# Performance work log

Measured on AMD Instinct MI355X. Metric: run time of the kernel, lower is better.

The kernel has to match this reference:

```python
import math
import jax, jax.numpy as jnp
import numpy as np

B, S, D, H = 4, 1024, 512, 8
DK = D // H


def lin(x, W, b):
    # torch nn.Linear: y = x @ W.T + b, W: [out, in]
    return jnp.einsum('...i,oi->...o', x, W) + b


def layer_norm(x, scale, bias, eps=1e-5):
    m = jnp.mean(x, axis=-1, keepdims=True)
    v = jnp.var(x, axis=-1, keepdims=True)
    return (x - m) / jnp.sqrt(v + eps) * scale + bias


def mha(q_in, k_in, v_in, Wq, bq, Wk, bk, Wv, bv, Wo, bo, gammas, mask, zero_pad):
    b, s, _ = q_in.shape
    q = lin(q_in, Wq, bq).reshape(b, s, H, DK).transpose(0, 2, 1, 3)  # bhsd
    k = lin(k_in, Wk, bk).reshape(b, s, H, DK).transpose(0, 2, 1, 3)
    v = lin(v_in, Wv, bv).reshape(b, s, H, DK).transpose(0, 2, 1, 3)
    scores = jnp.einsum('bhid,bhjd->bhij', q, k) / math.sqrt(DK)
    # no-grad distance-decay branch
    s_ = jnp.where(mask, scores, jnp.float32(-1e32))
    s_ = jax.nn.softmax(s_, axis=-1) * mask
    distcum = jnp.cumsum(s_, axis=-1)
    disttotal = jnp.sum(s_, axis=-1, keepdims=True)
    idx = jnp.arange(s)
    pos = jnp.abs(idx[None, :] - idx[:, None]).astype(jnp.float32)[None, None]  # |i-j|
    dist = jax.lax.stop_gradient(jnp.sqrt(jnp.clip((disttotal - distcum) * pos, 0.0, None)))
    gamma = -jax.nn.softplus(gammas)[None]  # [1,h,1,1]
    total_effect = jnp.clip(jnp.exp(dist * gamma), 1e-5, 1e5)
    scores = scores * total_effect
    # NOTE: original code calls scores.masked_fill(...) without assignment (no-op);
    # faithfully NOT re-masking before this softmax.
    att = jax.nn.softmax(scores, axis=-1)
    if zero_pad:
        att = att.at[:, :, 0, :].set(0.0)
    out = jnp.einsum('bhij,bhjd->bhid', att, v).transpose(0, 2, 1, 3).reshape(b, s, D)
    return lin(out, Wo, bo)


def setup_inputs() -> dict:
    key = jax.random.key(0)
    ks = jax.random.split(key, 32)
    ki = iter(range(32))

    def w(shape, scale=0.02):
        return jax.random.normal(ks[next(ki)], shape, jnp.float32) * scale

    inp = {
        'q_emb': jax.random.normal(ks[next(ki)], (B, S, D), jnp.float32),
        'qa_emb': jax.random.normal(ks[next(ki)], (B, S, D), jnp.float32),
    }
    for blk in (1, 2, 3):
        inp[f'Wq{blk}'] = w((D, D)); inp[f'bq{blk}'] = jnp.zeros((D,), jnp.float32)
        if blk == 3:
            inp['Wk3'] = w((D, D)); inp['bk3'] = jnp.zeros((D,), jnp.float32)
        inp[f'Wv{blk}'] = w((D, D)); inp[f'bv{blk}'] = jnp.zeros((D,), jnp.float32)
        inp[f'Wo{blk}'] = w((D, D)); inp[f'bo{blk}'] = jnp.zeros((D,), jnp.float32)
        inp[f'g{blk}'] = w((H, 1, 1), 0.5)
        inp[f'ls{blk}'] = jnp.ones((D,), jnp.float32)
        inp[f'lb{blk}'] = jnp.zeros((D,), jnp.float32)
    inp['know'] = jax.random.uniform(ks[next(ki)], (1, 1, D), jnp.float32, -1.0, 1.0)
    inp['Wlk'] = w((D, DK)); inp['b_lk'] = jnp.zeros((D,), jnp.float32)
    inp['Wlv'] = w((D, DK)); inp['b_lv'] = jnp.zeros((D,), jnp.float32)
    return inp


def reference(q_emb, qa_emb,
              Wq1, bq1, Wv1, bv1, Wo1, bo1, g1, ls1, lb1,
              Wq2, bq2, Wv2, bv2, Wo2, bo2, g2, ls2, lb2,
              Wq3, bq3, Wk3, bk3, Wv3, bv3, Wo3, bo3, g3, ls3, lb3,
              know, Wlk, b_lk, Wlv, b_lv):
    b, s, d = q_emb.shape
    ones = jnp.ones((s, s), dtype=bool)
    mask_peek = jnp.tril(ones, k=0)[None, None]   # peek_cur=True
    mask_nopeek = jnp.tril(ones, k=-1)[None, None]  # peek_cur=False

    # block1 / block2 share k and q projections (kq_same=True)
    hq = layer_norm(q_emb + mha(q_emb, q_emb, q_emb, Wq1, bq1, Wq1, bq1,
                                Wv1, bv1, Wo1, bo1, g1, mask_peek, False), ls1, lb1)
    ha = layer_norm(qa_emb + mha(qa_emb, qa_emb, qa_emb, Wq2, bq2, Wq2, bq2,
                                 Wv2, bv2, Wo2, bo2, g2, mask_peek, False), ls2, lb2)
    query = jnp.broadcast_to(know, (b, s, d))
    h = layer_norm(query + mha(query, hq, ha, Wq3, bq3, Wk3, bk3,
                               Wv3, bv3, Wo3, bo3, g3, mask_nopeek, True), ls3, lb3)

    # small multi-head combine
    key_t = jax.nn.sigmoid(lin(query.reshape(b, s, H, DK), Wlk, b_lk))  # [b,s,h,d]
    val_t = jax.nn.sigmoid(lin(h.reshape(b, s, H, DK), Wlv, b_lv))     # [b,s,h,d]
    beta = jnp.einsum('bshd,bsd->bsh', key_t, q_emb)
    alpha = jax.nn.softmax(beta, axis=-1)
    out = jnp.einsum('bsh,bshd->bsd', alpha, val_t)
    return out
```

## Files before the change

### kernel.cpp

```cpp
#include <hip/hip_runtime.h>
#include <math.h>

#define BB 4
#define S 1024
#define D 512
#define H 8
#define DKH 64

#define ATT_LD 1032
#define LOG2E 1.4426950408889634f

typedef __attribute__((ext_vector_type(8))) short bf16x8;
typedef __attribute__((ext_vector_type(4))) float f32x4;

#if __has_builtin(__builtin_amdgcn_exp2f)
#define EXP2(x) __builtin_amdgcn_exp2f(x)
#else
#define EXP2(x) exp2f(x)
#endif
#if __has_builtin(__builtin_amdgcn_sqrtf)
#define SQRTF(x) __builtin_amdgcn_sqrtf(x)
#else
#define SQRTF(x) sqrtf(x)
#endif
#if __has_builtin(__builtin_amdgcn_rcpf)
#define RCPF(x) __builtin_amdgcn_rcpf(x)
#else
#define RCPF(x) (1.0f / (x))
#endif

__device__ __forceinline__ unsigned short f2bf(float f){
  unsigned int u = __float_as_uint(f);
  u += 0x7FFFu + ((u >> 16) & 1u);
  return (unsigned short)(u >> 16);
}
__device__ __forceinline__ unsigned short f2bf_rhu(float f){
  return (unsigned short)((__float_as_uint(f) + 0x8000u) >> 16);
}
__device__ __forceinline__ unsigned int pk_rhu(float lo, float hi){
  unsigned int a = __float_as_uint(lo) + 0x8000u;
  unsigned int b = __float_as_uint(hi) + 0x8000u;
#if __has_builtin(__builtin_amdgcn_perm)
  return __builtin_amdgcn_perm(b, a, 0x07060302u);
#else
  return (a >> 16) | (b & 0xffff0000u);
#endif
}
__device__ __forceinline__ float bf2f(unsigned int v){
  return __uint_as_float(v << 16);
}
__device__ __forceinline__ f32x4 MFMA(bf16x8 a, bf16x8 b, f32x4 c){
  return __builtin_amdgcn_mfma_f32_16x16x32_bf16(a, b, c, 0, 0, 0);
}
__device__ __forceinline__ void gl_lds16(const void* g, void* l){
  __builtin_amdgcn_global_load_lds(
      (const __attribute__((address_space(1))) void*)g,
      (__attribute__((address_space(3))) void*)l, 16, 0, 0);
}

template<int CTRL>
__device__ __forceinline__ float dppadd(float v){
  int s = __builtin_amdgcn_update_dpp(0, __float_as_int(v), CTRL, 0xf, 0xf, true);
  return v + __int_as_float(s);
}
__device__ __forceinline__ float rdl(float v, int l){
  return __int_as_float(__builtin_amdgcn_readlane(__float_as_int(v), l));
}
__device__ __forceinline__ void wave_scan64(float v, int lane, float& incl, float& total){
  float r = dppadd<0x111>(v);
  r = dppadd<0x112>(r);
  r = dppadd<0x114>(r);
  r = dppadd<0x118>(r);
  float t0 = rdl(r, 15), t1 = rdl(r, 31), t2 = rdl(r, 47), t3 = rdl(r, 63);
  const int row = lane >> 4;
  float off = (row > 0 ? t0 : 0.f) + (row > 1 ? t1 : 0.f) + (row > 2 ? t2 : 0.f);
  incl = r + off;
  total = (t0 + t1) + (t2 + t3);
}
__device__ __forceinline__ float wave_sum64(float v){
  float r = dppadd<0x111>(v);
  r = dppadd<0x112>(r);
  r = dppadd<0x114>(r);
  r = dppadd<0x118>(r);
  return (rdl(r, 15) + rdl(r, 31)) + (rdl(r, 47) + rdl(r, 63));
}

__device__ __forceinline__ float blk_sum(float* r, int t, float v){
  r[t] = v; __syncthreads();
  for (int s = 128; s > 0; s >>= 1){
    if (t < s) r[t] += r[t + s];
    __syncthreads();
  }
  float res = r[0]; __syncthreads();
  return res;
}

struct GemmJobs {
  const unsigned short* A[4];
  const unsigned short* W[4];
  const float* bias[4];
  void* C[4];
};
template<int OUTBF>
__global__ __launch_bounds__(256) void mfma_gemm_b(GemmJobs jb)
{
  __shared__ __align__(16) short As[128][32];
  __shared__ __align__(16) short Ws[128][32];
  const int t = threadIdx.x;
  const int z = blockIdx.z;
  const int n0 = blockIdx.x * 128, m0 = blockIdx.y * 128;
  const unsigned short* A = jb.A[z];
  const unsigned short* W = jb.W[z];
  const float* bias = jb.bias[z];
  const int w = t >> 6, lane = t & 63;
  const int wm = (w >> 1) << 6, wn = (w & 1) << 6;
  const int lm = lane & 15, q = lane >> 4;
  const int r = t >> 2, cc = (t & 3) << 3;
  char* ldsA = ((char*)&As[0][0]) + w * 1024;
  char* ldsW = ((char*)&Ws[0][0]) + w * 1024;
  f32x4 acc[4][4];
  #pragma unroll
  for (int a_ = 0; a_ < 4; a_++)
    #pragma unroll
    for (int b_ = 0; b_ < 4; b_++)
      acc[a_][b_] = (f32x4){0.f, 0.f, 0.f, 0.f};
  for (int k0 = 0; k0 < D; k0 += 32){
    gl_lds16(&A[(size_t)(m0 + r)      * D + k0 + cc], ldsA);
    gl_lds16(&A[(size_t)(m0 + r + 64) * D + k0 + cc], ldsA + 4096);
    gl_lds16(&W[(size_t)(n0 + r)      * D + k0 + cc], ldsW);
    gl_lds16(&W[(size_t)(n0 + r + 64) * D + k0 + cc], ldsW + 4096);
    __syncthreads();
    bf16x8 af[4], bf[4];
    #pragma unroll
    for (int mt = 0; mt < 4; mt++) af[mt] = *(const bf16x8*)&As[wm + mt*16 + lm][q*8];
    #pragma unroll
    for (int nt = 0; nt < 4; nt++) bf[nt] = *(const bf16x8*)&Ws[wn + nt*16 + lm][q*8];
    #pragma unroll
    for (int mt = 0; mt < 4; mt++)
      #pragma unroll
      for (int nt = 0; nt < 4; nt++)
        acc[mt][nt] = MFMA(af[mt], bf[nt], acc[mt][nt]);
    __syncthreads();
  }
  #pragma unroll
  for (int nt = 0; nt < 4; nt++){
    const int n = n0 + wn + nt*16 + lm;
    const float bs = bias[n];
    #pragma unroll
    for (int mt = 0; mt < 4; mt++){
      const int mb = m0 + wm + mt*16 + (q << 2);
      f32x4 c = acc[mt][nt];
      #pragma unroll
      for (int rr = 0; rr < 4; rr++){
        float vv = c[rr] + bs;
        if (OUTBF)
          ((unsigned short*)jb.C[z])[(size_t)(mb + rr) * D + n] = f2bf(vv);
        else
          ((float*)jb.C[z])[(size_t)(mb + rr) * D + n] = vv;
      }
    }
  }
}

#define KS_LD 66
struct VTArgs { const unsigned short* v[2]; unsigned short* vt[2]; int nz; };
__global__ __launch_bounds__(256) void vt_kernel(VTArgs a)
{
  __shared__ unsigned short tile[64 * KS_LD];
  const int lin = blockIdx.x;
  const int xcd = lin & 7, slot = lin >> 3;
  const int j0 = (slot & 15) * 64;
  const int set = slot >> 4;
  const int z   = (a.nz == 2) ? (set & 1)  : 0;
  const int grp = (a.nz == 2) ? (set >> 1) : set;
  const int bh = xcd + 8 * grp, b = bh >> 3, h = bh & 7;
  const int t = threadIdx.x;
  const unsigned short* vp = a.v[z];
  unsigned short* vtp = a.vt[z] + (size_t)bh * 64 * S;
  #pragma unroll
  for (int p = 0; p < 2; p++){
    int lin2 = t + p * 256, row = lin2 >> 3, c8 = (lin2 & 7) << 3;
    *(uint4*)&tile[row * KS_LD + c8] =
      *(const uint4*)&vp[((size_t)b * S + j0 + row) * D + h * DKH + c8];
  }
  __syncthreads();
  #pragma unroll
  for (int p = 0; p < 2; p++){
    int lin2 = t + p * 256, d = lin2 >> 3, c8 = (lin2 & 7) << 3;
    unsigned short tmp[8];
    #pragma unroll
    for (int jx = 0; jx < 8; jx++) tmp[jx] = tile[(c8 + jx) * KS_LD + d];
    *(uint4*)&vtp[(size_t)d * S + j0 + c8] = *(const uint4*)tmp;
  }
}

struct FAArgs {
  const unsigned short* qk[2];
  const unsigned short* vt[2];
  unsigned short* ctx[2];
  const float* g[2];
  const float* c3;
  int diag, zero_pad, nz;
};
template<int C3>
__global__ __launch_bounds__(256, 4) void fused_attn(FAArgs a)
{
  __shared__ __align__(16) unsigned short att[16 * ATT_LD];
  __shared__ float ls2s[16];
  const int t = threadIdx.x;
  const int lin = blockIdx.x;
  const int xcd = lin & 7;
  const int slot = lin >> 3;
  const int i0 = (slot & 63) * 16;
  const int set = slot >> 6;
  const int z   = (a.nz == 2) ? (set & 1)  : 0;
  const int grp = (a.nz == 2) ? (set >> 1) : set;
  const int bh = xcd + 8 * grp, b = bh >> 3, h = bh & 7;
  const int w = t >> 6, lane = t & 63, lm = lane & 15, q = lane >> 4;
  const unsigned short* qkp = a.qk[z];
  const unsigned short* vtp = a.vt[z] + (size_t)bh * 64 * S;
  unsigned short* ctxp = a.ctx[z];
  float gm2;
  { float gv = a.g[z][h];
    gm2 = -((gv > 20.f) ? gv : log1pf(expf(gv))) * LOG2E; }

  if (!C3){
    const size_t rowbase = (size_t)b * S;
    bf16x8 af0 = *(const bf16x8*)&qkp[(rowbase + i0 + lm) * D + h * DKH + q*8];
    bf16x8 af1 = *(const bf16x8*)&qkp[(rowbase + i0 + lm) * D + h * DKH + 32 + q*8];
    size_t kb = (rowbase + w*16 + lm) * D + h * DKH;
    bf16x8 bv0 = *(const bf16x8*)&qkp[kb + q*8];
    bf16x8 bv1 = *(const bf16x8*)&qkp[kb + 32 + q*8];
    for (int jc = 0; jc < S; jc += 64){
      bf16x8 nb0, nb1;
      if (jc + 64 < S){
        size_t kb2 = (rowbase + jc + 64 + w*16 + lm) * D + h * DKH;
        nb0 = *(const bf16x8*)&qkp[kb2 + q*8];
        nb1 = *(const bf16x8*)&qkp[kb2 + 32 + q*8];
      }
      f32x4 acc = (f32x4){0.f, 0.f, 0.f, 0.f};
      acc = MFMA(af0, bv0, acc);
      acc = MFMA(af1, bv1, acc);
      #pragma unroll
      for (int rr = 0; rr < 4; rr++)
        att[(q*4 + rr) * ATT_LD + jc + w*16 + lm] = f2bf_rhu(acc[rr] * 0.125f);
      bv0 = nb0; bv1 = nb1;
    }
  }
  __syncthreads();

  const int jA0 = lane * 8, jB0 = 512 + lane * 8;

  float cH[16], erH[16];
  if (C3){
    const float* c3p = a.c3 + ((size_t)b * H + h) * S;
    #pragma unroll
    for (int sg = 0; sg < 2; sg++)
      #pragma unroll
      for (int p4 = 0; p4 < 2; p4++){
        float4 x = *(const float4*)&c3p[sg*512 + lane*8 + p4*4];
        cH[sg*8+p4*4+0] = x.x * LOG2E; cH[sg*8+p4*4+1] = x.y * LOG2E;
        cH[sg*8+p4*4+2] = x.z * LOG2E; cH[sg*8+p4*4+3] = x.w * LOG2E;
      }
    #pragma unroll
    for (int k = 0; k < 16; k++) erH[k] = EXP2(cH[k]);
  }

  auto decay_row = [&](const float (&c)[16], const float (&er)[16],
                       const int i, unsigned short* rowp, const int rl){
    const int jmax = i + a.diag;
    const bool skipB = (jmax < 512);
    float pl[16];
    float runA = 0.f;
    #pragma unroll
    for (int k = 0; k < 8; k++){
      float e = (jA0 + k <= jmax) ? er[k] : 0.f;
      runA += e; pl[k] = runA;
    }
    float sA, TA;
    wave_scan64(runA, lane, sA, TA);
    float T = TA, sB = 0.f, runB = 0.f;
    if (!skipB){
      #pragma unroll
      for (int k = 0; k < 8; k++){
        float e = (jB0 + k <= jmax) ? er[8+k] : 0.f;
        runB += e; pl[8+k] = runB;
      }
      float TB;
      wave_scan64(runB, lane, sB, TB);
      T = TA + TB;
    }
    const float inv1 = RCPF(T);
    const float cbaseA = (T - (sA - runA)) * inv1;
    const float fiA = (float)(i - jA0);
    float ls2 = 0.f;
    #pragma unroll
    for (int k = 0; k < 8; k++){
      float remn = fmaf(-pl[k], inv1, cbaseA);
      float pos  = fabsf(fiA - (float)k);
      float dist = SQRTF(fmaxf(remn * pos, 0.f));
      float eff  = fmaxf(EXP2(gm2 * dist), 1e-5f);
      float pp   = EXP2(c[k] * eff);
      ls2 += pp; pl[k] = pp;
    }
    if (!skipB){
      const float cbaseB = (T - (TA + sB - runB)) * inv1;
      const float fiB = (float)(i - jB0);
      #pragma unroll
      for (int k = 0; k < 8; k++){
        float remn = fmaf(-pl[8+k], inv1, cbaseB);
        float pos  = fabsf(fiB - (float)k);
        float dist = SQRTF(fmaxf(remn * pos, 0.f));
        float eff  = fmaxf(EXP2(gm2 * dist), 1e-5f);
        float pp   = EXP2(c[8+k] * eff);
        ls2 += pp; pl[8+k] = pp;
      }
    } else {
      #pragma unroll
      for (int k = 0; k < 8; k++){ pl[8+k] = er[8+k]; ls2 += er[8+k]; }
    }
    ls2 = wave_sum64(ls2);
    if (lane == 0) ls2s[rl] = RCPF(ls2);
    #pragma unroll
    for (int sg = 0; sg < 2; sg++){
      uint4 o;
      o.x = pk_rhu(pl[sg*8+0], pl[sg*8+1]);
      o.y = pk_rhu(pl[sg*8+2], pl[sg*8+3]);
      o.z = pk_rhu(pl[sg*8+4], pl[sg*8+5]);
      o.w = pk_rhu(pl[sg*8+6], pl[sg*8+7]);
      *(uint4*)&rowp[sg*512 + lane*8] = o;
    }
  };

  for (int rloc = 0; rloc < 4; rloc++){
    const int rl = w*4 + rloc;
    const int i = i0 + rl;
    unsigned short* rowp = &att[rl * ATT_LD];
    if (C3 && a.zero_pad && i == 0){
      uint4 zz = make_uint4(0u,0u,0u,0u);
      *(uint4*)&rowp[jA0] = zz;
      *(uint4*)&rowp[jB0] = zz;
      if (lane == 0) ls2s[0] = 1.f;
      continue;
    }
    if (C3){
      decay_row(cH, erH, i, rowp, rl);
    } else {
      float c[16], er[16];
      #pragma unroll
      for (int sg = 0; sg < 2; sg++){
        uint4 u = *(const uint4*)&rowp[sg*512 + lane*8];
        unsigned int uu[4] = {u.x, u.y, u.z, u.w};
        #pragma unroll
        for (int mel = 0; mel < 4; mel++){
          c[sg*8 + mel*2]     = bf2f(uu[mel] & 0xffffu) * LOG2E;
          c[sg*8 + mel*2 + 1] = bf2f(uu[mel] >> 16) * LOG2E;
        }
      }
      #pragma unroll
      for (int k = 0; k < 16; k++) er[k] = EXP2(c[k]);
      decay_row(c, er, i, rowp, rl);
    }
  }
  __syncthreads();

  f32x4 acc = (f32x4){0.f,0.f,0.f,0.f};
  const unsigned short* vrow = &vtp[(size_t)(w*16 + lm) * S];
  bf16x8 bv0 = *(const bf16x8*)&vrow[q*8];
  bf16x8 bv1 = *(const bf16x8*)&vrow[32 + q*8];
  for (int kc = 0; kc < S; kc += 64){
    bf16x8 nb0, nb1;
    if (kc + 64 < S){
      nb0 = *(const bf16x8*)&vrow[kc + 64 + q*8];
      nb1 = *(const bf16x8*)&vrow[kc + 96 + q*8];
    }
    bf16x8 a0 = *(const bf16x8*)&att[lm * ATT_LD + kc + q*8];
    bf16x8 a1 = *(const bf16x8*)&att[lm * ATT_LD + kc + 32 + q*8];
    acc = MFMA(a0, bv0, acc);
    acc = MFMA(a1, bv1, acc);
    bv0 = nb0; bv1 = nb1;
  }
  #pragma unroll
  for (int rr = 0; rr < 4; rr++){
    const int rl = q*4 + rr;
    const float sc = ls2s[rl];
    const int row = i0 + rl;
    ctxp[((size_t)b * S + row) * D + h * DKH + w*16 + lm] = f2bf(acc[rr] * sc);
  }
}

struct LNJobs {
  const float* resid[2];
  const float* y[2];
  const float* ls[2];
  const float* lb[2];
  unsigned short* out[2];
  int bcast[2];
};
__global__ __launch_bounds__(256) void ln_residual_b(LNJobs j)
{
  const int z = blockIdx.y;
  const int r = blockIdx.x, t = threadIdx.x;
  __shared__ float red[256];
  const size_t base = (size_t)r * D;
  const float* resid = j.resid[z];
  const float* y = j.y[z];
  const int bcast = j.bcast[z];
  float r0 = bcast ? resid[t]       : resid[base + t];
  float r1 = bcast ? resid[t + 256] : resid[base + t + 256];
  float x0 = r0 + y[base + t];
  float x1 = r1 + y[base + t + 256];
  float mean = blk_sum(red, t, x0 + x1) * (1.0f / 512.0f);
  float d0 = x0 - mean, d1 = x1 - mean;
  float var = blk_sum(red, t, d0*d0 + d1*d1) * (1.0f / 512.0f);
  float inv = rsqrtf(var + 1e-5f);
  j.out[z][base + t]       = f2bf(d0 * inv * j.ls[z][t]       + j.lb[z][t]);
  j.out[z][base + t + 256] = f2bf(d1 * inv * j.ls[z][t + 256] + j.lb[z][t + 256]);
}

struct CvtJobs {
  const float* s[12];
  unsigned short* d[12];
  int n[12];
};
__global__ __launch_bounds__(256) void cvt_all(CvtJobs jb){
  const int z = blockIdx.y;
  const int n = jb.n[z];
  const float* s = jb.s[z];
  unsigned short* d = jb.d[z];
  for (int idx = blockIdx.x * 256 + threadIdx.x; idx < n; idx += gridDim.x * 256)
    d[idx] = f2bf(s[idx]);
}

__global__ __launch_bounds__(256) void know_kernel(
    const float* __restrict__ know, const float* __restrict__ Wq3,
    const float* __restrict__ bq3, float* __restrict__ q3,
    const float* __restrict__ Wlk, const float* __restrict__ blk_,
    float* __restrict__ keyt)
{
  if (blockIdx.x < 128){
    const int wv = (blockIdx.x * 256 + threadIdx.x) >> 6;
    const int lane = threadIdx.x & 63;
    const float* wr = Wq3 + (size_t)wv * 512 + lane * 8;
    const float* kr = know + lane * 8;
    float4 w0 = *(const float4*)&wr[0], w1 = *(const float4*)&wr[4];
    float4 k0 = *(const float4*)&kr[0], k1 = *(const float4*)&kr[4];
    float p = w0.x*k0.x + w0.y*k0.y + w0.z*k0.z + w0.w*k0.w
            + w1.x*k1.x + w1.y*k1.y + w1.z*k1.z + w1.w*k1.w;
    p = wave_sum64(p);
    if (lane == 0) q3[wv] = p + bq3[wv];
  } else {
    int idx = (blockIdx.x - 128) * 256 + threadIdx.x;
    int h = idx >> 9, n = idx & 511;
    float acc = 0.f;
    for (int i = 0; i < 64; i++) acc += know[h * 64 + i] * Wlk[(size_t)n * 64 + i];
    keyt[idx] = 1.f / (1.f + __expf(-(acc + blk_[n])));
  }
}

__global__ __launch_bounds__(256) void scores3_kernel(
    const float* __restrict__ q3, const unsigned short* __restrict__ k3,
    float* __restrict__ c3)
{
  int idx = blockIdx.x * 256 + threadIdx.x;
  int j  = idx & (S - 1);
  int bh = idx >> 10;
  int h  = bh & 7, b = bh >> 3;
  const unsigned short* kp = k3 + ((size_t)b * S + j) * D + h * DKH;
  const float* qp = q3 + h * DKH;
  float acc = 0.f;
  #pragma unroll
  for (int d8 = 0; d8 < 64; d8 += 8){
    uint4 u = *(const uint4*)&kp[d8];
    unsigned int uu[4] = {u.x, u.y, u.z, u.w};
    #pragma unroll
    for (int mel = 0; mel < 4; mel++){
      acc += qp[d8 + 2*mel]     * bf2f(uu[mel] & 0xffffu);
      acc += qp[d8 + 2*mel + 1] * bf2f(uu[mel] >> 16);
    }
  }
  c3[idx] = acc * 0.125f;
}

__global__ __launch_bounds__(256) void alphas_kernel(
    const float* __restrict__ keyt, const float* __restrict__ q_emb,
    float* __restrict__ alpha)
{
  const int row = blockIdx.x * 4 + (threadIdx.x >> 6);
  const int l = threadIdx.x & 63;
  const int h = l >> 3, sub = l & 7;
  const float* qr = q_emb + (size_t)row * D;
  const float* kt = keyt + h * D;
  float p = 0.f;
  for (int d = sub; d < D; d += 8) p += kt[d] * qr[d];
  p += __shfl_xor(p, 1, 64);
  p += __shfl_xor(p, 2, 64);
  p += __shfl_xor(p, 4, 64);
  float m = p;
  m = fmaxf(m, __shfl_xor(m, 8, 64));
  m = fmaxf(m, __shfl_xor(m, 16, 64));
  m = fmaxf(m, __shfl_xor(m, 32, 64));
  float e = __expf(p - m);
  float ssum = e;
  ssum += __shfl_xor(ssum, 8, 64);
  ssum += __shfl_xor(ssum, 16, 64);
  ssum += __shfl_xor(ssum, 32, 64);
  if (sub == 0) alpha[(size_t)row * H + h] = e / ssum;
}

__global__ __launch_bounds__(256) void val_fused(
    const unsigned short* __restrict__ Ah,
    const unsigned short* __restrict__ Wv,
    const float* __restrict__ blv,
    const float* __restrict__ alpha,
    float* __restrict__ out)
{
  __shared__ __align__(16) short As[128][32];
  __shared__ __align__(16) short Ws[128][32];
  __shared__ float als[128];
  const int t = threadIdx.x;
  const int n0 = blockIdx.x * 128, m0 = blockIdx.y * 128;
  if (t < 128) als[t] = alpha[m0 + t];
  const int w = t >> 6, lane = t & 63;
  const int wm = (w >> 1) << 6, wn = (w & 1) << 6;
  const int lm = lane & 15, q = lane >> 4;
  const int r = t >> 2, cc = (t & 3) << 3;
  f32x4 acc[4][4];
  #pragma unroll
  for (int a_ = 0; a_ < 4; a_++)
    #pragma unroll
    for (int b_ = 0; b_ < 4; b_++)
      acc[a_][b_] = (f32x4){0.f, 0.f, 0.f, 0.f};
  for (int k0 = 0; k0 < 64; k0 += 32){
    *(uint4*)&As[r][cc]      = *(const uint4*)&Ah[(size_t)(m0 + r) * 64 + k0 + cc];
    *(uint4*)&As[r + 64][cc] = *(const uint4*)&Ah[(size_t)(m0 + r + 64) * 64 + k0 + cc];
    *(uint4*)&Ws[r][cc]      = *(const uint4*)&Wv[(size_t)(n0 + r) * 64 + k0 + cc];
    *(uint4*)&Ws[r + 64][cc] = *(const uint4*)&Wv[(size_t)(n0 + r + 64) * 64 + k0 + cc];
    __syncthreads();
    bf16x8 af[4], bf[4];
    #pragma unroll
    for (int mt = 0; mt < 4; mt++) af[mt] = *(const bf16x8*)&As[wm + mt*16 + lm][q*8];
    #pragma unroll
    for (int nt = 0; nt < 4; nt++) bf[nt] = *(const bf16x8*)&Ws[wn + nt*16 + lm][q*8];
    #pragma unroll
    for (int mt = 0; mt < 4; mt++)
      #pragma unroll
      for (int nt = 0; nt < 4; nt++)
        acc[mt][nt] = MFMA(af[mt], bf[nt], acc[mt][nt]);
    __syncthreads();
  }
  #pragma unroll
  for (int nt = 0; nt < 4; nt++){
    const int n = n0 + wn + nt*16 + lm;
    const float bs = blv[n];
    #pragma unroll
    for (int mt = 0; mt < 4; mt++){
      const int mb = m0 + wm + mt*16;
      f32x4 c = acc[mt][nt];
      float part = 0.f;
      #pragma unroll
      for (int rr = 0; rr < 4; rr++){
        const int ml = (mb - m0) + (q << 2) + rr;
        float sg = 1.f / (1.f + __expf(-(c[rr] + bs)));
        part += als[ml] * sg;
      }
      part += __shfl_xor(part, 16, 64);
      if ((q & 1) == 0){
        const int srow = (mb >> 3) + (q >> 1);
        out[(size_t)srow * D + n] = part;
      }
    }
  }
}

extern "C" void kernel_launch(void* const* d_in, const int* in_sizes, int n_in,
                              void* d_out, int out_size, void* d_ws, size_t ws_size,
                              hipStream_t stream) {
  const float* q_emb  = (const float*)d_in[0];
  const float* qa_emb = (const float*)d_in[1];
  const float* Wq1 = (const float*)d_in[2],  *bq1 = (const float*)d_in[3];
  const float* Wv1 = (const float*)d_in[4],  *bv1 = (const float*)d_in[5];
  const float* Wo1 = (const float*)d_in[6],  *bo1 = (const float*)d_in[7];
  const float* g1  = (const float*)d_in[8],  *ls1 = (const float*)d_in[9],  *lb1 = (const float*)d_in[10];
  const float* Wq2 = (const float*)d_in[11], *bq2 = (const float*)d_in[12];
  const float* Wv2 = (const float*)d_in[13], *bv2 = (const float*)d_in[14];
  const float* Wo2 = (const float*)d_in[15], *bo2 = (const float*)d_in[16];
  const float* g2  = (const float*)d_in[17], *ls2 = (const float*)d_in[18], *lb2 = (const float*)d_in[19];
  const float* Wq3 = (const float*)d_in[20], *bq3 = (const float*)d_in[21];
  const float* Wk3 = (const float*)d_in[22], *bk3 = (const float*)d_in[23];
  const float* Wv3 = (const float*)d_in[24], *bv3 = (const float*)d_in[25];
  const float* Wo3 = (const float*)d_in[26], *bo3 = (const float*)d_in[27];
  const float* g3  = (const float*)d_in[28], *ls3 = (const float*)d_in[29], *lb3 = (const float*)d_in[30];
  const float* know = (const float*)d_in[31];
  const float* Wlk  = (const float*)d_in[32], *b_lk = (const float*)d_in[33];
  const float* Wlv  = (const float*)d_in[34], *b_lv = (const float*)d_in[35];
  float* outp = (float*)d_out;

  const size_t NSD = (size_t)BB * S * D;
  unsigned short* p = (unsigned short*)d_ws;
  unsigned short* qk1b = p; p += NSD;
  unsigned short* v1b  = p; p += NSD;
  unsigned short* qk2b = p; p += NSD;
  unsigned short* v2b  = p; p += NSD;
  unsigned short* k3b  = p; p += NSD;
  unsigned short* v3b  = p; p += NSD;
  unsigned short* ctx1b= p; p += NSD;
  unsigned short* ctx2b= p; p += NSD;
  unsigned short* ctx3b= p; p += NSD;
  unsigned short* xqb  = p; p += NSD;
  unsigned short* xab  = p; p += NSD;
  unsigned short* hqb  = p; p += NSD;
  unsigned short* hab  = p; p += NSD;
  unsigned short* hfb  = p; p += NSD;
  unsigned short* vt1  = p; p += NSD;
  unsigned short* vt2  = p; p += NSD;
  unsigned short* vt3  = p; p += NSD;
  unsigned short* wb   = p; p += (size_t)9 * D * D;
  unsigned short* wlvb = p; p += (size_t)D * DKH;
  float* yv0   = (float*)p;
  float* yv1   = yv0 + NSD;
  float* q3    = yv1 + NSD;
  float* keyt  = q3 + 512;
  float* c3    = keyt + 4096;
  float* alpha = c3 + (size_t)BB * H * S;

  unsigned short* Wq1b = wb + 0*(size_t)D*D;
  unsigned short* Wv1b = wb + 1*(size_t)D*D;
  unsigned short* Wo1b = wb + 2*(size_t)D*D;
  unsigned short* Wq2b = wb + 3*(size_t)D*D;
  unsigned short* Wv2b = wb + 4*(size_t)D*D;
  unsigned short* Wo2b = wb + 5*(size_t)D*D;
  unsigned short* Wk3b = wb + 6*(size_t)D*D;
  unsigned short* Wv3b = wb + 7*(size_t)D*D;
  unsigned short* Wo3b = wb + 8*(size_t)D*D;

  CvtJobs jb;
  jb.s[0] = q_emb;  jb.d[0] = xqb;  jb.n[0] = (int)NSD;
  jb.s[1] = qa_emb; jb.d[1] = xab;  jb.n[1] = (int)NSD;
  jb.s[2] = Wq1; jb.d[2] = Wq1b; jb.n[2] = D*D;
  jb.s[3] = Wv1; jb.d[3] = Wv1b; jb.n[3] = D*D;
  jb.s[4] = Wo1; jb.d[4] = Wo1b; jb.n[4] = D*D;
  jb.s[5] = Wq2; jb.d[5] = Wq2b; jb.n[5] = D*D;
  jb.s[6] = Wv2; jb.d[6] = Wv2b; jb.n[6] = D*D;
  jb.s[7] = Wo2; jb.d[7] = Wo2b; jb.n[7] = D*D;
  jb.s[8] = Wk3; jb.d[8] = Wk3b; jb.n[8] = D*D;
  jb.s[9] = Wv3; jb.d[9] = Wv3b; jb.n[9] = D*D;
  jb.s[10] = Wo3; jb.d[10] = Wo3b; jb.n[10] = D*D;
  jb.s[11] = Wlv; jb.d[11] = wlvb; jb.n[11] = D*DKH;
  cvt_all<<<dim3(256, 12), 256, 0, stream>>>(jb);

  {
    GemmJobs g;
    g.A[0]=xqb; g.W[0]=Wq1b; g.bias[0]=bq1; g.C[0]=qk1b;
    g.A[1]=xqb; g.W[1]=Wv1b; g.bias[1]=bv1; g.C[1]=v1b;
    g.A[2]=xab; g.W[2]=Wq2b; g.bias[2]=bq2; g.C[2]=qk2b;
    g.A[3]=xab; g.W[3]=Wv2b; g.bias[3]=bv2; g.C[3]=v2b;
    mfma_gemm_b<1><<<dim3(4, 32, 4), 256, 0, stream>>>(g);
  }
  { VTArgs a; a.v[0]=v1b; a.v[1]=v2b; a.vt[0]=vt1; a.vt[1]=vt2; a.nz=2;
    vt_kernel<<<dim3(1024), 256, 0, stream>>>(a); }
  { FAArgs a;
    a.qk[0]=qk1b; a.qk[1]=qk2b; a.vt[0]=vt1; a.vt[1]=vt2;
    a.ctx[0]=ctx1b; a.ctx[1]=ctx2b; a.g[0]=g1; a.g[1]=g2;
    a.c3=nullptr; a.diag=0; a.zero_pad=0; a.nz=2;
    fused_attn<0><<<dim3(4096), 256, 0, stream>>>(a); }
  {
    GemmJobs g;
    g.A[0]=ctx1b; g.W[0]=Wo1b; g.bias[0]=bo1; g.C[0]=yv0;
    g.A[1]=ctx2b; g.W[1]=Wo2b; g.bias[1]=bo2; g.C[1]=yv1;
    g.A[2]=ctx1b; g.W[2]=Wo1b; g.bias[2]=bo1; g.C[2]=yv0;
    g.A[3]=ctx1b; g.W[3]=Wo1b; g.bias[3]=bo1; g.C[3]=yv0;
    mfma_gemm_b<0><<<dim3(4, 32, 2), 256, 0, stream>>>(g);
  }
  {
    LNJobs lj;
    lj.resid[0]=q_emb;  lj.y[0]=yv0; lj.ls[0]=ls1; lj.lb[0]=lb1; lj.out[0]=hqb; lj.bcast[0]=0;
    lj.resid[1]=qa_emb; lj.y[1]=yv1; lj.ls[1]=ls2; lj.lb[1]=lb2; lj.out[1]=hab; lj.bcast[1]=0;
    ln_residual_b<<<dim3(BB*S, 2), 256, 0, stream>>>(lj);
  }

  know_kernel<<<144, 256, 0, stream>>>(know, Wq3, bq3, q3, Wlk, b_lk, keyt);
  {
    GemmJobs g;
    g.A[0]=hqb; g.W[0]=Wk3b; g.bias[0]=bk3; g.C[0]=k3b;
    g.A[1]=hab; g.W[1]=Wv3b; g.bias[1]=bv3; g.C[1]=v3b;
    g.A[2]=hqb; g.W[2]=Wk3b; g.bias[2]=bk3; g.C[2]=k3b;
    g.A[3]=hqb; g.W[3]=Wk3b; g.bias[3]=bk3; g.C[3]=k3b;
    mfma_gemm_b<1><<<dim3(4, 32, 2), 256, 0, stream>>>(g);
  }
  { VTArgs a; a.v[0]=v3b; a.v[1]=v3b; a.vt[0]=vt3; a.vt[1]=vt3; a.nz=1;
    vt_kernel<<<dim3(512), 256, 0, stream>>>(a); }
  scores3_kernel<<<128, 256, 0, stream>>>(q3, k3b, c3);
  { FAArgs a;
    a.qk[0]=k3b; a.qk[1]=k3b; a.vt[0]=vt3; a.vt[1]=vt3;
    a.ctx[0]=ctx3b; a.ctx[1]=ctx3b; a.g[0]=g3; a.g[1]=g3;
    a.c3=c3; a.diag=-1; a.zero_pad=1; a.nz=1;
    fused_attn<1><<<dim3(2048), 256, 0, stream>>>(a); }
  {
    GemmJobs g;
    g.A[0]=ctx3b; g.W[0]=Wo3b; g.bias[0]=bo3; g.C[0]=yv0;
    g.A[1]=ctx3b; g.W[1]=Wo3b; g.bias[1]=bo3; g.C[1]=yv0;
    g.A[2]=ctx3b; g.W[2]=Wo3b; g.bias[2]=bo3; g.C[2]=yv0;
    g.A[3]=ctx3b; g.W[3]=Wo3b; g.bias[3]=bo3; g.C[3]=yv0;
    mfma_gemm_b<0><<<dim3(4, 32, 1), 256, 0, stream>>>(g);
  }
  {
    LNJobs lj;
    lj.resid[0]=know; lj.y[0]=yv0; lj.ls[0]=ls3; lj.lb[0]=lb3; lj.out[0]=hfb; lj.bcast[0]=1;
    lj.resid[1]=know; lj.y[1]=yv0; lj.ls[1]=ls3; lj.lb[1]=lb3; lj.out[1]=hfb; lj.bcast[1]=1;
    ln_residual_b<<<dim3(BB*S, 1), 256, 0, stream>>>(lj);
  }

  alphas_kernel<<<1024, 256, 0, stream>>>(keyt, q_emb, alpha);
  val_fused<<<dim3(4, 256), 256, 0, stream>>>(hfb, wlvb, b_lv, alpha, outp);
}
```

Measured before the change: 436.4 us.

## Precompute shared prefix-sum table for block-3 decay and deepen K/V prefetch

For the block-3 attention path (C3), the scores depend only on the column, so the exp prefix sums are computed once per block into a padded shared-memory table. Each row then looks up its total and per-column cumulative values instead of running per-row wave scans. The QK and PV loops also prefetch two chunks ahead instead of one, and the non-C3 path is inlined with exponentials computed lazily. The cost is extra shared memory and register pressure, which may affect occupancy at 4 blocks per CU.

```diff
diff --git a/kernel.cpp b/kernel.cpp
--- a/kernel.cpp
+++ b/kernel.cpp
@@ -9,6 +9,7 @@
 
 #define ATT_LD 1032
 #define LOG2E 1.4426950408889634f
+#define PIDX(j) ((j) + ((j) >> 3))
 
 typedef __attribute__((ext_vector_type(8))) short bf16x8;
 typedef __attribute__((ext_vector_type(4))) float f32x4;
@@ -207,6 +208,7 @@
 {
   __shared__ __align__(16) unsigned short att[16 * ATT_LD];
   __shared__ float ls2s[16];
+  __shared__ float Ptab[1152];
   const int t = threadIdx.x;
   const int lin = blockIdx.x;
   const int xcd = lin & 7;
@@ -228,109 +230,63 @@
     const size_t rowbase = (size_t)b * S;
     bf16x8 af0 = *(const bf16x8*)&qkp[(rowbase + i0 + lm) * D + h * DKH + q*8];
     bf16x8 af1 = *(const bf16x8*)&qkp[(rowbase + i0 + lm) * D + h * DKH + 32 + q*8];
-    size_t kb = (rowbase + w*16 + lm) * D + h * DKH;
-    bf16x8 bv0 = *(const bf16x8*)&qkp[kb + q*8];
-    bf16x8 bv1 = *(const bf16x8*)&qkp[kb + 32 + q*8];
+    size_t k0a = (rowbase + 0  + w*16 + lm) * D + h * DKH;
+    size_t k1a = (rowbase + 64 + w*16 + lm) * D + h * DKH;
+    bf16x8 c0a = *(const bf16x8*)&qkp[k0a + q*8];
+    bf16x8 c0b = *(const bf16x8*)&qkp[k0a + 32 + q*8];
+    bf16x8 c1a = *(const bf16x8*)&qkp[k1a + q*8];
+    bf16x8 c1b = *(const bf16x8*)&qkp[k1a + 32 + q*8];
     for (int jc = 0; jc < S; jc += 64){
-      bf16x8 nb0, nb1;
-      if (jc + 64 < S){
-        size_t kb2 = (rowbase + jc + 64 + w*16 + lm) * D + h * DKH;
-        nb0 = *(const bf16x8*)&qkp[kb2 + q*8];
-        nb1 = *(const bf16x8*)&qkp[kb2 + 32 + q*8];
+      bf16x8 na, nb;
+      if (jc + 128 < S){
+        size_t kb2 = (rowbase + jc + 128 + w*16 + lm) * D + h * DKH;
+        na = *(const bf16x8*)&qkp[kb2 + q*8];
+        nb = *(const bf16x8*)&qkp[kb2 + 32 + q*8];
       }
       f32x4 acc = (f32x4){0.f, 0.f, 0.f, 0.f};
-      acc = MFMA(af0, bv0, acc);
-      acc = MFMA(af1, bv1, acc);
+      acc = MFMA(af0, c0a, acc);
+      acc = MFMA(af1, c0b, acc);
       #pragma unroll
       for (int rr = 0; rr < 4; rr++)
         att[(q*4 + rr) * ATT_LD + jc + w*16 + lm] = f2bf_rhu(acc[rr] * 0.125f);
-      bv0 = nb0; bv1 = nb1;
+      c0a = c1a; c0b = c1b; c1a = na; c1b = nb;
     }
   }
-  __syncthreads();
-
-  const int jA0 = lane * 8, jB0 = 512 + lane * 8;
-
-  float cH[16], erH[16];
+
+  float cHA[8], cHB[8];
   if (C3){
     const float* c3p = a.c3 + ((size_t)b * H + h) * S;
-    #pragma unroll
-    for (int sg = 0; sg < 2; sg++)
-      #pragma unroll
-      for (int p4 = 0; p4 < 2; p4++){
-        float4 x = *(const float4*)&c3p[sg*512 + lane*8 + p4*4];
-        cH[sg*8+p4*4+0] = x.x * LOG2E; cH[sg*8+p4*4+1] = x.y * LOG2E;
-        cH[sg*8+p4*4+2] = x.z * LOG2E; cH[sg*8+p4*4+3] = x.w * LOG2E;
-      }
-    #pragma unroll
-    for (int k = 0; k < 16; k++) erH[k] = EXP2(cH[k]);
-  }
-
-  auto decay_row = [&](const float (&c)[16], const float (&er)[16],
-                       const int i, unsigned short* rowp, const int rl){
-    const int jmax = i + a.diag;
-    const bool skipB = (jmax < 512);
-    float pl[16];
-    float runA = 0.f;
-    #pragma unroll
-    for (int k = 0; k < 8; k++){
-      float e = (jA0 + k <= jmax) ? er[k] : 0.f;
-      runA += e; pl[k] = runA;
+    if (w == 0){
+      float e[16]; float run = 0.f;
+      float4 f0 = *(const float4*)&c3p[lane*16];
+      float4 f1 = *(const float4*)&c3p[lane*16 + 4];
+      float4 f2 = *(const float4*)&c3p[lane*16 + 8];
+      float4 f3 = *(const float4*)&c3p[lane*16 + 12];
+      e[0]=f0.x; e[1]=f0.y; e[2]=f0.z; e[3]=f0.w;
+      e[4]=f1.x; e[5]=f1.y; e[6]=f1.z; e[7]=f1.w;
+      e[8]=f2.x; e[9]=f2.y; e[10]=f2.z; e[11]=f2.w;
+      e[12]=f3.x; e[13]=f3.y; e[14]=f3.z; e[15]=f3.w;
+      float loc[16];
+      #pragma unroll
+      for (int k = 0; k < 16; k++){ run += EXP2(e[k] * LOG2E); loc[k] = run; }
+      float incl, tot;
+      wave_scan64(run, lane, incl, tot);
+      const float off = incl - run;
+      #pragma unroll
+      for (int k = 0; k < 16; k++) Ptab[PIDX(lane*16 + k)] = loc[k] + off;
     }
-    float sA, TA;
-    wave_scan64(runA, lane, sA, TA);
-    float T = TA, sB = 0.f, runB = 0.f;
-    if (!skipB){
-      #pragma unroll
-      for (int k = 0; k < 8; k++){
-        float e = (jB0 + k <= jmax) ? er[8+k] : 0.f;
-        runB += e; pl[8+k] = runB;
-      }
-      float TB;
-      wave_scan64(runB, lane, sB, TB);
-      T = TA + TB;
-    }
-    const float inv1 = RCPF(T);
-    const float cbaseA = (T - (sA - runA)) * inv1;
-    const float fiA = (float)(i - jA0);
-    float ls2 = 0.f;
-    #pragma unroll
-    for (int k = 0; k < 8; k++){
-      float remn = fmaf(-pl[k], inv1, cbaseA);
-      float pos  = fabsf(fiA - (float)k);
-      float dist = SQRTF(fmaxf(remn * pos, 0.f));
-      float eff  = fmaxf(EXP2(gm2 * dist), 1e-5f);
-      float pp   = EXP2(c[k] * eff);
-      ls2 += pp; pl[k] = pp;
-    }
-    if (!skipB){
-      const float cbaseB = (T - (TA + sB - runB)) * inv1;
-      const float fiB = (float)(i - jB0);
-      #pragma unroll
-      for (int k = 0; k < 8; k++){
-        float remn = fmaf(-pl[8+k], inv1, cbaseB);
-        float pos  = fabsf(fiB - (float)k);
-        float dist = SQRTF(fmaxf(remn * pos, 0.f));
-        float eff  = fmaxf(EXP2(gm2 * dist), 1e-5f);
-        float pp   = EXP2(c[8+k] * eff);
-        ls2 += pp; pl[8+k] = pp;
-      }
-    } else {
-      #pragma unroll
-      for (int k = 0; k < 8; k++){ pl[8+k] = er[8+k]; ls2 += er[8+k]; }
-    }
-    ls2 = wave_sum64(ls2);
-    if (lane == 0) ls2s[rl] = RCPF(ls2);
-    #pragma unroll
-    for (int sg = 0; sg < 2; sg++){
-      uint4 o;
-      o.x = pk_rhu(pl[sg*8+0], pl[sg*8+1]);
-      o.y = pk_rhu(pl[sg*8+2], pl[sg*8+3]);
-      o.z = pk_rhu(pl[sg*8+4], pl[sg*8+5]);
-      o.w = pk_rhu(pl[sg*8+6], pl[sg*8+7]);
-      *(uint4*)&rowp[sg*512 + lane*8] = o;
-    }
-  };
+    float4 x0 = *(const float4*)&c3p[lane*8];
+    float4 x1 = *(const float4*)&c3p[lane*8 + 4];
+    float4 y0 = *(const float4*)&c3p[512 + lane*8];
+    float4 y1 = *(const float4*)&c3p[512 + lane*8 + 4];
+    cHA[0]=x0.x*LOG2E; cHA[1]=x0.y*LOG2E; cHA[2]=x0.z*LOG2E; cHA[3]=x0.w*LOG2E;
+    cHA[4]=x1.x*LOG2E; cHA[5]=x1.y*LOG2E; cHA[6]=x1.z*LOG2E; cHA[7]=x1.w*LOG2E;
+    cHB[0]=y0.x*LOG2E; cHB[1]=y0.y*LOG2E; cHB[2]=y0.z*LOG2E; cHB[3]=y0.w*LOG2E;
+    cHB[4]=y1.x*LOG2E; cHB[5]=y1.y*LOG2E; cHB[6]=y1.z*LOG2E; cHB[7]=y1.w*LOG2E;
+  }
+  __syncthreads();
+
+  const int jA0 = lane * 8, jB0 = 512 + lane * 8;
 
   for (int rloc = 0; rloc < 4; rloc++){
     const int rl = w*4 + rloc;
@@ -343,42 +299,137 @@
       if (lane == 0) ls2s[0] = 1.f;
       continue;
     }
+    const int jmax = i + a.diag;
+    float pl[16];
+    float ls2 = 0.f;
+
     if (C3){
-      decay_row(cH, erH, i, rowp, rl);
+      const float T = Ptab[PIDX(jmax)];
+      const float inv1 = RCPF(T);
+      const float fiA = (float)(i - jA0);
+      const float fiB = (float)(i - jB0);
+      #pragma unroll
+      for (int k = 0; k < 8; k++){
+        const int j = jA0 + k;
+        const int jc2 = (j < jmax) ? j : jmax;
+        float Pj = Ptab[PIDX(jc2)];
+        float remn = (T - Pj) * inv1;
+        float pos  = fabsf(fiA - (float)k);
+        float dist = SQRTF(fmaxf(remn * pos, 0.f));
+        float eff  = fmaxf(EXP2(gm2 * dist), 1e-5f);
+        float pp   = EXP2(cHA[k] * eff);
+        ls2 += pp; pl[k] = pp;
+      }
+      #pragma unroll
+      for (int k = 0; k < 8; k++){
+        const int j = jB0 + k;
+        const int jc2 = (j < jmax) ? j : jmax;
+        float Pj = Ptab[PIDX(jc2)];
+        float remn = (T - Pj) * inv1;
+        float pos  = fabsf(fiB - (float)k);
+        float dist = SQRTF(fmaxf(remn * pos, 0.f));
+        float eff  = fmaxf(EXP2(gm2 * dist), 1e-5f);
+        float pp   = EXP2(cHB[k] * eff);
+        ls2 += pp; pl[8+k] = pp;
+      }
     } else {
-      float c[16], er[16];
-      #pragma unroll
-      for (int sg = 0; sg < 2; sg++){
-        uint4 u = *(const uint4*)&rowp[sg*512 + lane*8];
-        unsigned int uu[4] = {u.x, u.y, u.z, u.w};
+      const bool skipB = (jmax < 512);
+      float cA[8], cB[8];
+      uint4 uAv = *(const uint4*)&rowp[jA0];
+      uint4 uBv = *(const uint4*)&rowp[jB0];
+      unsigned int ua[4] = {uAv.x, uAv.y, uAv.z, uAv.w};
+      unsigned int ub[4] = {uBv.x, uBv.y, uBv.z, uBv.w};
+      #pragma unroll
+      for (int mel = 0; mel < 4; mel++){
+        cA[mel*2]     = bf2f(ua[mel] & 0xffffu) * LOG2E;
+        cA[mel*2 + 1] = bf2f(ua[mel] >> 16) * LOG2E;
+        cB[mel*2]     = bf2f(ub[mel] & 0xffffu) * LOG2E;
+        cB[mel*2 + 1] = bf2f(ub[mel] >> 16) * LOG2E;
+      }
+      float runA = 0.f;
+      #pragma unroll
+      for (int k = 0; k < 8; k++){
+        float e = (jA0 + k <= jmax) ? EXP2(cA[k]) : 0.f;
+        runA += e; pl[k] = runA;
+      }
+      float sA, TA;
+      wave_scan64(runA, lane, sA, TA);
+      float T = TA, sB = 0.f, runB = 0.f, TB = 0.f;
+      if (!skipB){
         #pragma unroll
-        for (int mel = 0; mel < 4; mel++){
-          c[sg*8 + mel*2]     = bf2f(uu[mel] & 0xffffu) * LOG2E;
-          c[sg*8 + mel*2 + 1] = bf2f(uu[mel] >> 16) * LOG2E;
+        for (int k = 0; k < 8; k++){
+          float e = (jB0 + k <= jmax) ? EXP2(cB[k]) : 0.f;
+          runB += e; pl[8+k] = runB;
         }
-      }
-      #pragma unroll
-      for (int k = 0; k < 16; k++) er[k] = EXP2(c[k]);
-      decay_row(c, er, i, rowp, rl);
+        wave_scan64(runB, lane, sB, TB);
+        T = TA + TB;
+      }
+      const float inv1 = RCPF(T);
+      const float cbaseA = (T - (sA - runA)) * inv1;
+      const float fiA = (float)(i - jA0);
+      #pragma unroll
+      for (int k = 0; k < 8; k++){
+        float remn = fmaf(-pl[k], inv1, cbaseA);
+        float pos  = fabsf(fiA - (float)k);
+        float dist = SQRTF(fmaxf(remn * pos, 0.f));
+        float eff  = fmaxf(EXP2(gm2 * dist), 1e-5f);
+        float pp   = EXP2(cA[k] * eff);
+        ls2 += pp; pl[k] = pp;
+      }
+      if (!skipB){
+        const float cbaseB = (T - (TA + sB - runB)) * inv1;
+        const float fiB = (float)(i - jB0);
+        #pragma unroll
+        for (int k = 0; k < 8; k++){
+          float remn = fmaf(-pl[8+k], inv1, cbaseB);
+          float pos  = fabsf(fiB - (float)k);
+          float dist = SQRTF(fmaxf(remn * pos, 0.f));
+          float eff  = fmaxf(EXP2(gm2 * dist), 1e-5f);
+          float pp   = EXP2(cB[k] * eff);
+          ls2 += pp; pl[8+k] = pp;
+        }
+      } else {
+        #pragma unroll
+        for (int k = 0; k < 8; k++){
+          float e2 = EXP2(cB[k]);
+          pl[8+k] = e2; ls2 += e2;
+        }
+      }
     }
+
+    ls2 = wave_sum64(ls2);
+    if (lane == 0) ls2s[rl] = RCPF(ls2);
+    uint4 oA, oB;
+    oA.x = pk_rhu(pl[0], pl[1]);
+    oA.y = pk_rhu(pl[2], pl[3]);
+    oA.z = pk_rhu(pl[4], pl[5]);
+    oA.w = pk_rhu(pl[6], pl[7]);
+    oB.x = pk_rhu(pl[8], pl[9]);
+    oB.y = pk_rhu(pl[10], pl[11]);
+    oB.z = pk_rhu(pl[12], pl[13]);
+    oB.w = pk_rhu(pl[14], pl[15]);
+    *(uint4*)&rowp[jA0] = oA;
+    *(uint4*)&rowp[jB0] = oB;
   }
   __syncthreads();
 
   f32x4 acc = (f32x4){0.f,0.f,0.f,0.f};
   const unsigned short* vrow = &vtp[(size_t)(w*16 + lm) * S];
-  bf16x8 bv0 = *(const bf16x8*)&vrow[q*8];
-  bf16x8 bv1 = *(const bf16x8*)&vrow[32 + q*8];
+  bf16x8 p0a = *(const bf16x8*)&vrow[q*8];
+  bf16x8 p0b = *(const bf16x8*)&vrow[32 + q*8];
+  bf16x8 p1a = *(const bf16x8*)&vrow[64 + q*8];
+  bf16x8 p1b = *(const bf16x8*)&vrow[96 + q*8];
   for (int kc = 0; kc < S; kc += 64){
-    bf16x8 nb0, nb1;
-    if (kc + 64 < S){
-      nb0 = *(const bf16x8*)&vrow[kc + 64 + q*8];
-      nb1 = *(const bf16x8*)&vrow[kc + 96 + q*8];
+    bf16x8 na, nb;
+    if (kc + 128 < S){
+      na = *(const bf16x8*)&vrow[kc + 128 + q*8];
+      nb = *(const bf16x8*)&vrow[kc + 160 + q*8];
     }
     bf16x8 a0 = *(const bf16x8*)&att[lm * ATT_LD + kc + q*8];
     bf16x8 a1 = *(const bf16x8*)&att[lm * ATT_LD + kc + 32 + q*8];
-    acc = MFMA(a0, bv0, acc);
-    acc = MFMA(a1, bv1, acc);
-    bv0 = nb0; bv1 = nb1;
+    acc = MFMA(a0, p0a, acc);
+    acc = MFMA(a1, p0b, acc);
+    p0a = p1a; p0b = p1b; p1a = na; p1b = nb;
   }
   #pragma unroll
   for (int rr = 0; rr < 4; rr++){
```

New measurement: 435.8 us. About the same (-0.1%).
